# Kernel tuning notes

Measured on AMD Instinct MI355X. Metric: run time of the kernel, lower is better.

Reference implementation:

```python
import jax, jax.numpy as jnp
import numpy as np

BLOCK = 128
FP8_MAX = 448.0


def _quantize_weight_blockwise(w):
    """Blockwise fp8 quantization of weight [O, I] -> (fp8-valued f32 weight, [O/B, I/B] scales)."""
    O, I = w.shape
    wb = w.reshape(O // BLOCK, BLOCK, I // BLOCK, BLOCK)
    amax = jnp.maximum(jnp.max(jnp.abs(wb), axis=(1, 3), keepdims=True), 1e-12)
    scale = amax / FP8_MAX  # [O/B,1,I/B,1]
    w_fp8 = (wb / scale).astype(jnp.float8_e4m3fn).astype(jnp.float32).reshape(O, I)
    return w_fp8, scale[:, 0, :, 0]


def setup_inputs() -> dict:
    key = jax.random.key(0)
    k1, k2 = jax.random.split(key)
    tokens, input_size, output_size = 8192, 4096, 4096
    x = jax.random.normal(k1, (tokens, input_size), dtype=jnp.float32)
    w_hp = jax.random.normal(k2, (output_size, input_size), dtype=jnp.float32) * 0.02
    weight, weight_scale_inv = _quantize_weight_blockwise(w_hp)
    return {"x": x, "weight": weight, "weight_scale_inv": weight_scale_inv}


def reference(x, weight, weight_scale_inv):
    # --- dynamic per-token fp8 quantization of activations ---
    amax = jnp.maximum(jnp.max(jnp.abs(x), axis=-1, keepdims=True), 1e-12)  # [T,1]
    x_scale = amax / FP8_MAX                                                # [T,1] f32
    x_fp8 = (x / x_scale).astype(jnp.float8_e4m3fn).astype(jnp.float32)     # fp8-valued f32
    # --- blockwise dequant of fp8 weight with weight_scale_inv ---
    O, I = weight.shape
    scale_full = jnp.repeat(jnp.repeat(weight_scale_inv, BLOCK, axis=0), BLOCK, axis=1)  # [O,I]
    w_deq = weight * scale_full
    # --- fp8 block-scaled GEMM (dequantized-equivalent math) ---
    y = jnp.einsum('tk,ok->to', x_fp8, w_deq) * x_scale  # [T, O]
    return y
```

## Files before the change

### kernel.cpp

```cpp
#include <hip/hip_runtime.h>
#include <stdint.h>

#define FP8_MAX 448.0f
#define TOKENS  8192
#define IDIM    4096
#define ODIM    4096

typedef float f32x4 __attribute__((ext_vector_type(4)));
typedef int   i32x4 __attribute__((ext_vector_type(4)));
typedef int   i32x8 __attribute__((ext_vector_type(8)));

__device__ __forceinline__ void async_copy16(const uint8_t* g, uint8_t* l) {
  __builtin_amdgcn_global_load_lds((const __attribute__((address_space(1))) void*)g,
                                   (__attribute__((address_space(3))) void*)l,
                                   16, 0, 0);
}

__global__ __launch_bounds__(256) void prep_kernel(
    const float* __restrict__ x, const float* __restrict__ w,
    uint8_t* __restrict__ xq, uint8_t* __restrict__ wq, float* __restrict__ xsc) {
  const int lane = threadIdx.x & 63;
  const int wid  = threadIdx.x >> 6;

  if (blockIdx.x < 2048) {
    const int row = blockIdx.x * 4 + wid;
    const f32x4* xr = (const f32x4*)(x + (size_t)row * IDIM);

    f32x4 v[16];
    float amax = 0.0f;
    #pragma unroll
    for (int k = 0; k < 16; k++) {
      v[k] = xr[lane + k * 64];
      amax = fmaxf(amax, fmaxf(fmaxf(fabsf(v[k].x), fabsf(v[k].y)),
                               fmaxf(fabsf(v[k].z), fabsf(v[k].w))));
    }
    #pragma unroll
    for (int off = 32; off > 0; off >>= 1)
      amax = fmaxf(amax, __shfl_xor(amax, off, 64));
    amax = fmaxf(amax, 1e-12f);
    const float scale = amax / FP8_MAX;
    if (lane == 0) xsc[row] = scale;

    uint32_t* out = (uint32_t*)(xq + (size_t)row * IDIM);
    #pragma unroll
    for (int k = 0; k < 16; k++) {
      float a = v[k].x / scale, b = v[k].y / scale;
      float c = v[k].z / scale, d = v[k].w / scale;
      int p = __builtin_amdgcn_cvt_pk_fp8_f32(a, b, 0, false);
      p = __builtin_amdgcn_cvt_pk_fp8_f32(c, d, p, true);
      out[lane + k * 64] = (uint32_t)p;
    }
  } else {
    const int row = (blockIdx.x - 2048) * 4 + wid;
    const f32x4* wp = (const f32x4*)(w + (size_t)row * IDIM);
    uint32_t* out = (uint32_t*)(wq + (size_t)row * IDIM);
    #pragma unroll
    for (int k = 0; k < 16; k++) {
      f32x4 t = wp[lane + k * 64];
      int p = __builtin_amdgcn_cvt_pk_fp8_f32(t.x, t.y, 0, false);
      p = __builtin_amdgcn_cvt_pk_fp8_f32(t.z, t.w, p, true);
      out[lane + k * 64] = (uint32_t)p;
    }
  }
}

__global__ __launch_bounds__(256) void gemm_fp8_kernel(
    const uint8_t* __restrict__ xq, const uint8_t* __restrict__ wq,
    const float* __restrict__ xsc, const float* __restrict__ wsi,
    float* __restrict__ y) {
  __shared__ __align__(16) uint8_t As0[128 * 128];
  __shared__ __align__(16) uint8_t Bs0[128 * 128];
  __shared__ __align__(16) uint8_t As1[128 * 128];
  __shared__ __align__(16) uint8_t Bs1[128 * 128];

  const int tid  = threadIdx.x;
  const int bid  = (blockIdx.x & 7) * 256 + (blockIdx.x >> 3);
  const int bo   = bid & 31;
  const int bt   = bid >> 5;
  const int t0   = bt << 7;
  const int o0   = bo << 7;
  const int lane = tid & 63;
  const int wave = tid >> 6;
  const int wr   = (wave >> 1) << 6;
  const int wc   = (wave & 1) << 6;
  const int ln   = lane & 15;
  const int quad = lane >> 4;

  const int rb  = tid >> 3;
  const int cs  = ((tid & 7) ^ (rb & 7)) << 4;
  const int lds = tid << 4;

  const int c0 = quad << 1;
  int aoff[4][2], boff[4][2];
  #pragma unroll
  for (int i = 0; i < 4; i++) {
    const int ra = wr + i * 16 + ln;
    const int sa = ra & 7;
    aoff[i][0] = ra * 128 + ((c0 ^ sa) << 4);
    aoff[i][1] = ra * 128 + (((c0 + 1) ^ sa) << 4);
    const int rb2 = wc + i * 16 + ln;
    const int sb = rb2 & 7;
    boff[i][0] = rb2 * 128 + ((c0 ^ sb) << 4);
    boff[i][1] = rb2 * 128 + (((c0 + 1) ^ sb) << 4);
  }

  f32x4 outer[4][4];
  #pragma unroll
  for (int i = 0; i < 4; i++)
    #pragma unroll
    for (int j = 0; j < 4; j++)
      outer[i][j] = (f32x4)(0.0f);

  const float* wsrow = wsi + bo * 32;
  const int ident = 0x7f7f7f7f;
  const f32x4 zero4 = (f32x4)(0.0f);

  auto stage = [&](uint8_t* Ad, uint8_t* Bd, int kb) {
    const int k0 = kb << 7;
    #pragma unroll
    for (int u = 0; u < 4; u++) {
      async_copy16(xq + ((size_t)(t0 + u * 32 + rb) << 12) + (k0 + cs),
                   Ad + u * 4096 + lds);
      async_copy16(wq + ((size_t)(o0 + u * 32 + rb) << 12) + (k0 + cs),
                   Bd + u * 4096 + lds);
    }
  };

  auto compute = [&](const uint8_t* Ab, const uint8_t* Bb, float s) {
    i32x8 a[4], b[4];
    #pragma unroll
    for (int i = 0; i < 4; i++) {
      i32x4 alo = *(const i32x4*)(Ab + aoff[i][0]);
      i32x4 ahi = *(const i32x4*)(Ab + aoff[i][1]);
      a[i] = __builtin_shufflevector(alo, ahi, 0, 1, 2, 3, 4, 5, 6, 7);
      i32x4 blo = *(const i32x4*)(Bb + boff[i][0]);
      i32x4 bhi = *(const i32x4*)(Bb + boff[i][1]);
      b[i] = __builtin_shufflevector(blo, bhi, 0, 1, 2, 3, 4, 5, 6, 7);
    }
    #pragma unroll
    for (int i = 0; i < 4; i++)
      #pragma unroll
      for (int j = 0; j < 4; j++) {
        f32x4 t = __builtin_amdgcn_mfma_scale_f32_16x16x128_f8f6f4(
            a[i], b[j], zero4, 0, 0, 0, ident, 0, ident);
        outer[i][j] += s * t;
      }
  };

  stage(As0, Bs0, 0);
  __syncthreads();

  for (int kb = 0; kb < 32; kb += 2) {
    if (kb + 1 < 32) stage(As1, Bs1, kb + 1);
    compute(As0, Bs0, wsrow[kb]);
    __syncthreads();

    if (kb + 2 < 32) stage(As0, Bs0, kb + 2);
    compute(As1, Bs1, wsrow[kb + 1]);
    __syncthreads();
  }

  #pragma unroll
  for (int i = 0; i < 4; i++) {
    #pragma unroll
    for (int r = 0; r < 4; r++) {
      const int t = t0 + wr + i * 16 + quad * 4 + r;
      const float sc = xsc[t];
      float* yp = y + ((size_t)t << 12) + o0 + wc + ln;
      #pragma unroll
      for (int j = 0; j < 4; j++)
        yp[j * 16] = outer[i][j][r] * sc;
    }
  }
}

extern "C" void kernel_launch(void* const* d_in, const int* in_sizes, int n_in,
                              void* d_out, int out_size, void* d_ws, size_t ws_size,
                              hipStream_t stream) {
  const float* x   = (const float*)d_in[0];
  const float* w   = (const float*)d_in[1];
  const float* wsi = (const float*)d_in[2];
  float* y = (float*)d_out;

  uint8_t* xq = (uint8_t*)d_ws;
  uint8_t* wq = xq + (size_t)TOKENS * IDIM;
  float*  xsc = (float*)(wq + (size_t)ODIM * IDIM);

  prep_kernel<<<3072, 256, 0, stream>>>(x, w, xq, wq, xsc);
  gemm_fp8_kernel<<<2048, 256, 0, stream>>>(xq, wq, xsc, wsi, y);
}
```

Measured before the change: 452.0 us.

## Enlarge FP8 GEMM tile to 256x256 with 8 waves and explicit barrier scheduling

Grows the GEMM block tile from 128x128 to 256x256 with 512 threads, so each wave computes a 128x64 sub-tile split into two halves per k-step. The aim is to raise data reuse per byte staged into LDS and to cut global traffic. It replaces __syncthreads with raw s_barrier, sched_barrier and s_setprio so that next-tile async loads overlap the MFMA bursts. The grid is now 512 blocks without the old block-index swizzle. The cost is 128KB of LDS per block, higher accumulator register pressure, and fewer blocks to spread across CUs.

```diff
diff --git a/kernel.cpp b/kernel.cpp
--- a/kernel.cpp
+++ b/kernel.cpp
@@ -14,6 +14,12 @@
   __builtin_amdgcn_global_load_lds((const __attribute__((address_space(1))) void*)g,
                                    (__attribute__((address_space(3))) void*)l,
                                    16, 0, 0);
+}
+
+__device__ __forceinline__ i32x8 ldfrag(const uint8_t* p, int o0, int o1) {
+  i32x4 lo = *(const i32x4*)(p + o0);
+  i32x4 hi = *(const i32x4*)(p + o1);
+  return __builtin_shufflevector(lo, hi, 0, 1, 2, 3, 4, 5, 6, 7);
 }
 
 __global__ __launch_bounds__(256) void prep_kernel(
@@ -64,79 +70,78 @@
   }
 }
 
-__global__ __launch_bounds__(256) void gemm_fp8_kernel(
+__global__ __launch_bounds__(512, 2) void gemm_fp8_kernel(
     const uint8_t* __restrict__ xq, const uint8_t* __restrict__ wq,
     const float* __restrict__ xsc, const float* __restrict__ wsi,
     float* __restrict__ y) {
-  __shared__ __align__(16) uint8_t As0[128 * 128];
-  __shared__ __align__(16) uint8_t Bs0[128 * 128];
-  __shared__ __align__(16) uint8_t As1[128 * 128];
-  __shared__ __align__(16) uint8_t Bs1[128 * 128];
+  __shared__ __align__(16) uint8_t As0[32768];
+  __shared__ __align__(16) uint8_t Bs0[32768];
+  __shared__ __align__(16) uint8_t As1[32768];
+  __shared__ __align__(16) uint8_t Bs1[32768];
 
   const int tid  = threadIdx.x;
-  const int bid  = (blockIdx.x & 7) * 256 + (blockIdx.x >> 3);
-  const int bo   = bid & 31;
-  const int bt   = bid >> 5;
-  const int t0   = bt << 7;
-  const int o0   = bo << 7;
+  const int bo   = blockIdx.x & 15;
+  const int bt   = blockIdx.x >> 4;
+  const int t0   = bt << 8;
+  const int o0   = bo << 8;
   const int lane = tid & 63;
-  const int wave = tid >> 6;
-  const int wr   = (wave >> 1) << 6;
-  const int wc   = (wave & 1) << 6;
+  const int wv   = tid >> 6;
+  const int wr   = (wv >> 2) << 7;
+  const int wc   = (wv & 3) << 6;
   const int ln   = lane & 15;
   const int quad = lane >> 4;
 
   const int rb  = tid >> 3;
   const int cs  = ((tid & 7) ^ (rb & 7)) << 4;
-  const int lds = tid << 4;
-
-  const int c0 = quad << 1;
-  int aoff[4][2], boff[4][2];
+  const int dst = tid << 4;
+
+  const int c0   = quad << 1;
+  const int sw   = ln & 7;
+  const int sw0  = ((c0    ) ^ sw) << 4;
+  const int sw1  = ((c0 + 1) ^ sw) << 4;
+  const int ab   = (wr + ln) * 128;
+  const int bb   = (wc + ln) * 128;
+
+  f32x4 outer[8][4];
   #pragma unroll
-  for (int i = 0; i < 4; i++) {
-    const int ra = wr + i * 16 + ln;
-    const int sa = ra & 7;
-    aoff[i][0] = ra * 128 + ((c0 ^ sa) << 4);
-    aoff[i][1] = ra * 128 + (((c0 + 1) ^ sa) << 4);
-    const int rb2 = wc + i * 16 + ln;
-    const int sb = rb2 & 7;
-    boff[i][0] = rb2 * 128 + ((c0 ^ sb) << 4);
-    boff[i][1] = rb2 * 128 + (((c0 + 1) ^ sb) << 4);
-  }
-
-  f32x4 outer[4][4];
-  #pragma unroll
-  for (int i = 0; i < 4; i++)
+  for (int i = 0; i < 8; i++)
     #pragma unroll
     for (int j = 0; j < 4; j++)
       outer[i][j] = (f32x4)(0.0f);
 
-  const float* wsrow = wsi + bo * 32;
+  const float* wsrow = wsi + (bo * 2 + (wc >> 7)) * 32;
   const int ident = 0x7f7f7f7f;
   const f32x4 zero4 = (f32x4)(0.0f);
 
-  auto stage = [&](uint8_t* Ad, uint8_t* Bd, int kb) {
-    const int k0 = kb << 7;
-    #pragma unroll
-    for (int u = 0; u < 4; u++) {
-      async_copy16(xq + ((size_t)(t0 + u * 32 + rb) << 12) + (k0 + cs),
-                   Ad + u * 4096 + lds);
-      async_copy16(wq + ((size_t)(o0 + u * 32 + rb) << 12) + (k0 + cs),
-                   Bd + u * 4096 + lds);
-    }
+  auto stageA = [&](uint8_t* Aw, int k0) {
+    #pragma unroll
+    for (int u = 0; u < 4; u++)
+      async_copy16(xq + ((size_t)(t0 + u * 64 + rb) << 12) + (k0 + cs),
+                   Aw + u * 8192 + dst);
   };
-
-  auto compute = [&](const uint8_t* Ab, const uint8_t* Bb, float s) {
+  auto stageB = [&](uint8_t* Bw, int k0) {
+    #pragma unroll
+    for (int u = 0; u < 4; u++)
+      async_copy16(wq + ((size_t)(o0 + u * 64 + rb) << 12) + (k0 + cs),
+                   Bw + u * 8192 + dst);
+  };
+
+  auto tile = [&](const uint8_t* Ar, const uint8_t* Br, uint8_t* Aw, uint8_t* Bw,
+                  int kb, bool doStage) {
+    const float s = wsrow[kb];
+    const int kn = (kb + 1) << 7;
     i32x8 a[4], b[4];
-    #pragma unroll
-    for (int i = 0; i < 4; i++) {
-      i32x4 alo = *(const i32x4*)(Ab + aoff[i][0]);
-      i32x4 ahi = *(const i32x4*)(Ab + aoff[i][1]);
-      a[i] = __builtin_shufflevector(alo, ahi, 0, 1, 2, 3, 4, 5, 6, 7);
-      i32x4 blo = *(const i32x4*)(Bb + boff[i][0]);
-      i32x4 bhi = *(const i32x4*)(Bb + boff[i][1]);
-      b[i] = __builtin_shufflevector(blo, bhi, 0, 1, 2, 3, 4, 5, 6, 7);
-    }
+
+    #pragma unroll
+    for (int i = 0; i < 4; i++)
+      a[i] = ldfrag(Ar + ab + i * 2048, sw0, sw1);
+    #pragma unroll
+    for (int j = 0; j < 4; j++)
+      b[j] = ldfrag(Br + bb + j * 2048, sw0, sw1);
+    if (doStage) { stageA(Aw, kn); stageB(Bw, kn); }
+    __builtin_amdgcn_s_barrier();
+    __builtin_amdgcn_sched_barrier(0);
+    __builtin_amdgcn_s_setprio(1);
     #pragma unroll
     for (int i = 0; i < 4; i++)
       #pragma unroll
@@ -145,23 +150,43 @@
             a[i], b[j], zero4, 0, 0, 0, ident, 0, ident);
         outer[i][j] += s * t;
       }
+    __builtin_amdgcn_s_setprio(0);
+    __builtin_amdgcn_s_barrier();
+    __builtin_amdgcn_sched_barrier(0);
+
+    #pragma unroll
+    for (int i = 0; i < 4; i++)
+      a[i] = ldfrag(Ar + ab + 8192 + i * 2048, sw0, sw1);
+    __builtin_amdgcn_s_barrier();
+    __builtin_amdgcn_sched_barrier(0);
+    __builtin_amdgcn_s_setprio(1);
+    #pragma unroll
+    for (int i = 0; i < 4; i++)
+      #pragma unroll
+      for (int j = 0; j < 4; j++) {
+        f32x4 t = __builtin_amdgcn_mfma_scale_f32_16x16x128_f8f6f4(
+            a[i], b[j], zero4, 0, 0, 0, ident, 0, ident);
+        outer[i + 4][j] += s * t;
+      }
+    __builtin_amdgcn_s_setprio(0);
+    asm volatile("s_waitcnt vmcnt(0)" ::: "memory");
+    __builtin_amdgcn_s_barrier();
+    __builtin_amdgcn_sched_barrier(0);
   };
 
-  stage(As0, Bs0, 0);
-  __syncthreads();
-
+  stageA(As0, 0); stageB(Bs0, 0);
+  asm volatile("s_waitcnt vmcnt(0)" ::: "memory");
+  __builtin_amdgcn_s_barrier();
+  __builtin_amdgcn_sched_barrier(0);
+
+  #pragma unroll 1
   for (int kb = 0; kb < 32; kb += 2) {
-    if (kb + 1 < 32) stage(As1, Bs1, kb + 1);
-    compute(As0, Bs0, wsrow[kb]);
-    __syncthreads();
-
-    if (kb + 2 < 32) stage(As0, Bs0, kb + 2);
-    compute(As1, Bs1, wsrow[kb + 1]);
-    __syncthreads();
+    tile(As0, Bs0, As1, Bs1, kb, true);
+    tile(As1, Bs1, As0, Bs0, kb + 1, kb + 1 < 31);
   }
 
   #pragma unroll
-  for (int i = 0; i < 4; i++) {
+  for (int i = 0; i < 8; i++) {
     #pragma unroll
     for (int r = 0; r < 4; r++) {
       const int t = t0 + wr + i * 16 + quad * 4 + r;
@@ -187,5 +212,5 @@
   float*  xsc = (float*)(wq + (size_t)ODIM * IDIM);
 
   prep_kernel<<<3072, 256, 0, stream>>>(x, w, xq, wq, xsc);
-  gemm_fp8_kernel<<<2048, 256, 0, stream>>>(xq, wq, xsc, wsi, y);
-}
+  gemm_fp8_kernel<<<(TOKENS / 256) * (ODIM / 256), 512, 0, stream>>>(xq, wq, xsc, wsi, y);
+}
```

Result: slower. 1.081 ms (+139.1%).
